# Optimization experiments

Measured on AMD Instinct MI355X. Metric: run time of the kernel, lower is better.

## Reference

```python
import jax, jax.numpy as jnp
import numpy as np

NUM_HEADS = 6

def setup_inputs() -> dict:
    key = jax.random.key(0)
    k1, k2, k3, k4 = jax.random.split(key, 4)
    B, T, C = 128, 256, 384
    s = 1.0 / np.sqrt(C)
    return {
        'x': jax.random.normal(k1, (B, T, C), dtype=jnp.float32),
        'Wq': jax.random.normal(k2, (C, C), dtype=jnp.float32) * s,
        'Wk': jax.random.normal(k3, (C, C), dtype=jnp.float32) * s,
        'Wv': jax.random.normal(k4, (C, C), dtype=jnp.float32) * s,
    }

def reference(x, Wq, Wk, Wv):
    B, T, C = x.shape
    H = NUM_HEADS
    d = C // H
    # projections (bias-free Linear), split into heads
    q = (x @ Wq).reshape(B, T, H, d)
    k = (x @ Wk).reshape(B, T, H, d)
    v = (x @ Wv).reshape(B, T, H, d)
    # NOTE: original scales by 1/sqrt(C), not 1/sqrt(head_dim)
    scale = 1.0 / jnp.sqrt(jnp.asarray(C, dtype=x.dtype))
    att = jnp.einsum('bqhd,bkhd->bhqk', q, k) * scale  # [B,H,T,T]
    causal = jnp.tril(jnp.ones((T, T), dtype=bool))
    att = jnp.where(causal, att, -jnp.inf)
    att = jax.nn.softmax(att, axis=-1)
    # dropout is identity in eval/deterministic mode
    out = jnp.einsum('bhqk,bkhd->bqhd', att, v)  # [B,T,H,d]
    return out.reshape(B, T, C)
```

## Files before the change

kernel.cpp:

```cpp
#include <hip/hip_runtime.h>


typedef unsigned short u16;
typedef float f32x4 __attribute__((ext_vector_type(4)));
typedef short s16x8 __attribute__((ext_vector_type(8)));

static constexpr int BB = 128;
static constexpr int TT = 256;
static constexpr int CC = 384;
static constexpr int HH = 6;
static constexpr int DD = 64;
static constexpr int MM = BB * TT;

static constexpr size_t WTOFF = 0;
static constexpr size_t XOFF  = (size_t)3 * CC * CC;

static constexpr float CSC = 0.07362242194579907f;

__device__ __forceinline__ u16 f2bf(float f) {
  unsigned u = __float_as_uint(f);
  u += 0x7fffu + ((u >> 16) & 1u);
  return (u16)(u >> 16);
}

__device__ __forceinline__ void g2l16(const u16* g, u16* l) {
  __builtin_amdgcn_global_load_lds(
      (const __attribute__((address_space(1))) u16*)g,
      (__attribute__((address_space(3))) u16*)l, 16, 0, 0);
}

__global__ void prep(const float* __restrict__ X, const float* __restrict__ Wq,
                     const float* __restrict__ Wk, const float* __restrict__ Wv,
                     u16* __restrict__ ws) {
  int bx = blockIdx.x;
  if (bx < 6144) {
    size_t i = (size_t)(bx * 256 + threadIdx.x) * 8;
    f32x4 a0 = *(const f32x4*)(X + i);
    f32x4 a1 = *(const f32x4*)(X + i + 4);
    s16x8 ab;
#pragma unroll
    for (int j = 0; j < 4; ++j) { ab[j] = (short)f2bf(a0[j]); ab[4 + j] = (short)f2bf(a1[j]); }
    *(s16x8*)(ws + XOFF + i) = ab;
  } else {
    int j = bx - 6144;
    int z = j / 576;
    const float* W = (z == 0) ? Wq : (z == 1) ? Wk : Wv;
    const float sc = (z == 0) ? CSC : 1.0f;
    u16* WT = ws + WTOFF + (size_t)z * CC * CC;
    int i = (j % 576) * 256 + threadIdx.x;
    int k = i / CC, n = i % CC;
    WT[(size_t)n * CC + k] = f2bf(W[i] * sc);
  }
}

__global__ __launch_bounds__(512, 2) void fused(const u16* __restrict__ ws,
                                                float* __restrict__ out) {
  const int bid = blockIdx.x;
  const int xc = bid & 7;
  const int g5 = bid >> 3;
  const int b = xc * 16 + g5 / 6;
  const int h = g5 % 6;

  __shared__ u16 Xs[256][64];
  __shared__ u16 Ws[192][64];
  __shared__ u16 Ks[256][64];
  __shared__ u16 VTs[64][256];

  const int tid = threadIdx.x;
  const int lane = tid & 63;
  const int w = tid >> 6;
  const int quad = lane >> 4;
  const int col = lane & 15;

  const u16* Xg = ws + XOFF + (size_t)b * TT * CC;
  const u16* Wg = ws + WTOFF;

  const int rl = lane >> 3;
  const int gb = (lane & 7) ^ rl;

  const int wm = (w >> 1) * 64;
  const int wn = (w & 1) * 96;

  f32x4 acc[4][6] = {};

  for (int kt = 0; kt < 6; ++kt) {
    if (kt) __syncthreads();
#pragma unroll
    for (int i = 0; i < 4; ++i) {
      int r0 = w * 32 + i * 8;
      g2l16(Xg + (size_t)(r0 + rl) * CC + kt * 64 + gb * 8, &Xs[r0][0]);
    }
#pragma unroll
    for (int i = 0; i < 3; ++i) {
      int r0 = w * 24 + i * 8;
      int rr = r0 + rl;
      int z = rr >> 6, nn = rr & 63;
      g2l16(Wg + (size_t)(z * CC + h * DD + nn) * CC + kt * 64 + gb * 8, &Ws[r0][0]);
    }
    __syncthreads();

    s16x8 af[4][2];
#pragma unroll
    for (int mt = 0; mt < 4; ++mt)
#pragma unroll
      for (int ks = 0; ks < 2; ++ks)
        af[mt][ks] = *(const s16x8*)(&Xs[wm + mt * 16 + col]
                                        [(((ks * 4 + quad) ^ (col & 7)) * 8)]);
#pragma unroll
    for (int nt = 0; nt < 6; ++nt) {
      s16x8 bf[2];
#pragma unroll
      for (int ks = 0; ks < 2; ++ks)
        bf[ks] = *(const s16x8*)(&Ws[wn + nt * 16 + col]
                                    [(((ks * 4 + quad) ^ (col & 7)) * 8)]);
#pragma unroll
      for (int ks = 0; ks < 2; ++ks)
#pragma unroll
        for (int mt = 0; mt < 4; ++mt)
          acc[mt][nt] = __builtin_amdgcn_mfma_f32_16x16x32_bf16(
              af[mt][ks], bf[ks], acc[mt][nt], 0, 0, 0);
    }
  }
  __syncthreads();

#pragma unroll
  for (int mt = 0; mt < 4; ++mt) {
    int tokb = wm + mt * 16 + quad * 4;
#pragma unroll
    for (int nt = 0; nt < 6; ++nt) {
      int gn = wn + nt * 16 + col;
      if (gn < 128) {
        u16* dst = (gn < 64) ? (u16*)Xs : (u16*)Ks;
        int d = gn & 63;
#pragma unroll
        for (int r = 0; r < 4; ++r) {
          int tok = tokb + r;
          dst[tok * 64 + (d ^ ((tok & 7) << 3))] = f2bf(acc[mt][nt][r]);
        }
      } else {
        int d = gn - 128;
        uint2 pk;
        pk.x = (unsigned)f2bf(acc[mt][nt][0]) | ((unsigned)f2bf(acc[mt][nt][1]) << 16);
        pk.y = (unsigned)f2bf(acc[mt][nt][2]) | ((unsigned)f2bf(acc[mt][nt][3]) << 16);
        *(uint2*)((u16*)VTs + d * 256 + (tokb ^ ((d & 15) << 3))) = pk;
      }
    }
  }
  __syncthreads();

  u16* Ps = (u16*)Ws + (size_t)w * 1152 + (size_t)col * 72;

  s16x8 qf[2][2];
#pragma unroll
  for (int gi = 0; gi < 2; ++gi) {
    int g = gi ? (15 - w) : w;
    int q = g * 16 + col;
#pragma unroll
    for (int ks = 0; ks < 2; ++ks)
      qf[gi][ks] = *(const s16x8*)((u16*)Xs + q * 64 +
                                   (((ks * 4 + quad) ^ (q & 7)) << 3));
  }

  f32x4 o[2][4] = {};
  float mst[2] = {-1.0e30f, -1.0e30f}, lst[2] = {0.0f, 0.0f};

  const int kthi = (15 - w) >> 2;
  for (int kt = 0; kt <= kthi; ++kt) {
    s16x8 kf[4][2], vf[4][2];
#pragma unroll
    for (int nt = 0; nt < 4; ++nt)
#pragma unroll
      for (int ks = 0; ks < 2; ++ks) {
        int key = kt * 64 + nt * 16 + col;
        kf[nt][ks] = *(const s16x8*)((u16*)Ks + key * 64 +
                                     (((ks * 4 + quad) ^ (key & 7)) << 3));
        int d = nt * 16 + col;
        vf[nt][ks] = *(const s16x8*)((u16*)VTs + d * 256 +
                                     ((kt * 64 + ks * 32 + quad * 8) ^ ((d & 15) << 3)));
      }

#pragma unroll
    for (int gi = 0; gi < 2; ++gi) {
      const int g = gi ? (15 - w) : w;
      const int gmax = g >> 2;
      if (kt > gmax) continue;

      f32x4 s[4] = {};
#pragma unroll
      for (int ks = 0; ks < 2; ++ks)
#pragma unroll
        for (int nt = 0; nt < 4; ++nt)
          s[nt] = __builtin_amdgcn_mfma_f32_16x16x32_bf16(kf[nt][ks], qf[gi][ks],
                                                          s[nt], 0, 0, 0);

      const int qq = (g & 3) * 16 + col;
      const bool diag = (kt == gmax);
      float rmax = -1.0e30f;
#pragma unroll
      for (int nt = 0; nt < 4; ++nt)
#pragma unroll
        for (int r = 0; r < 4; ++r) {
          float t = s[nt][r];
          if (diag && (nt * 16 + quad * 4 + r) > qq) t = -1.0e30f;
          s[nt][r] = t;
          rmax = fmaxf(rmax, t);
        }
      rmax = fmaxf(rmax, __shfl_xor(rmax, 16));
      rmax = fmaxf(rmax, __shfl_xor(rmax, 32));

      float mn = fmaxf(mst[gi], rmax);
      float alpha = exp2f(mst[gi] - mn);
      mst[gi] = mn;

      float lsum = 0.0f;
      unsigned pk[4][2];
#pragma unroll
      for (int nt = 0; nt < 4; ++nt) {
        float p0 = exp2f(s[nt][0] - mn), p1 = exp2f(s[nt][1] - mn);
        float p2 = exp2f(s[nt][2] - mn), p3 = exp2f(s[nt][3] - mn);
        lsum += (p0 + p1) + (p2 + p3);
        pk[nt][0] = (unsigned)f2bf(p0) | ((unsigned)f2bf(p1) << 16);
        pk[nt][1] = (unsigned)f2bf(p2) | ((unsigned)f2bf(p3) << 16);
      }
      lst[gi] = lst[gi] * alpha + lsum;

#pragma unroll
      for (int dt = 0; dt < 4; ++dt)
#pragma unroll
        for (int r = 0; r < 4; ++r) o[gi][dt][r] *= alpha;

      asm volatile("s_waitcnt lgkmcnt(0)" ::: "memory");
#pragma unroll
      for (int nt = 0; nt < 4; ++nt)
        *(uint2*)(Ps + nt * 16 + quad * 4) = make_uint2(pk[nt][0], pk[nt][1]);
      asm volatile("s_waitcnt lgkmcnt(0)" ::: "memory");

      s16x8 pf[2];
#pragma unroll
      for (int ks = 0; ks < 2; ++ks)
        pf[ks] = *(const s16x8*)(Ps + ks * 32 + quad * 8);

#pragma unroll
      for (int ks = 0; ks < 2; ++ks)
#pragma unroll
        for (int dt = 0; dt < 4; ++dt)
          o[gi][dt] = __builtin_amdgcn_mfma_f32_16x16x32_bf16(vf[dt][ks], pf[ks],
                                                              o[gi][dt], 0, 0, 0);
    }
  }

#pragma unroll
  for (int gi = 0; gi < 2; ++gi) {
    int g = gi ? (15 - w) : w;
    float l = lst[gi];
    l += __shfl_xor(l, 16);
    l += __shfl_xor(l, 32);
    float inv = 1.0f / l;
    int q = g * 16 + col;
#pragma unroll
    for (int dt = 0; dt < 4; ++dt) {
      f32x4 res;
#pragma unroll
      for (int r = 0; r < 4; ++r) res[r] = o[gi][dt][r] * inv;
      *(f32x4*)(out + (size_t)(b * TT + q) * CC + h * DD + dt * 16 + quad * 4) = res;
    }
  }
}

extern "C" void kernel_launch(void* const* d_in, const int* in_sizes, int n_in,
                              void* d_out, int out_size, void* d_ws, size_t ws_size,
                              hipStream_t stream) {
  const float* x  = (const float*)d_in[0];
  const float* wq = (const float*)d_in[1];
  const float* wk = (const float*)d_in[2];
  const float* wv = (const float*)d_in[3];
  u16* ws  = (u16*)d_ws;
  float* out = (float*)d_out;

  prep<<<dim3(6144 + 1728), 256, 0, stream>>>(x, wq, wk, wv, ws);
  fused<<<dim3(BB * HH), 512, 0, stream>>>(ws, out);
}
```

Baseline: 159.6 us.

## Double threads per block, pipeline projection loads, tile weight transpose via LDS

New measurement: 167.2 us. 4.7% more time.

```diff
diff --git a/kernel.cpp b/kernel.cpp
--- a/kernel.cpp
+++ b/kernel.cpp
@@ -4,6 +4,7 @@
 typedef unsigned short u16;
 typedef float f32x4 __attribute__((ext_vector_type(4)));
 typedef short s16x8 __attribute__((ext_vector_type(8)));
+typedef u16 u16x4 __attribute__((ext_vector_type(4)));
 
 static constexpr int BB = 128;
 static constexpr int TT = 256;
@@ -42,27 +43,43 @@
     for (int j = 0; j < 4; ++j) { ab[j] = (short)f2bf(a0[j]); ab[4 + j] = (short)f2bf(a1[j]); }
     *(s16x8*)(ws + XOFF + i) = ab;
   } else {
+    __shared__ u16 Lt[64][66];
     int j = bx - 6144;
-    int z = j / 576;
+    int z = j / 36, t = j % 36, ti = t / 6, tj = t % 6;
     const float* W = (z == 0) ? Wq : (z == 1) ? Wk : Wv;
     const float sc = (z == 0) ? CSC : 1.0f;
     u16* WT = ws + WTOFF + (size_t)z * CC * CC;
-    int i = (j % 576) * 256 + threadIdx.x;
-    int k = i / CC, n = i % CC;
-    WT[(size_t)n * CC + k] = f2bf(W[i] * sc);
-  }
-}
-
-__global__ __launch_bounds__(512, 2) void fused(const u16* __restrict__ ws,
-                                                float* __restrict__ out) {
+    const int rl = threadIdx.x >> 4;
+    const int cl = (threadIdx.x & 15) * 4;
+#pragma unroll
+    for (int it = 0; it < 4; ++it) {
+      int r = it * 16 + rl;
+      f32x4 v = *(const f32x4*)(W + (size_t)(ti * 64 + r) * CC + tj * 64 + cl);
+#pragma unroll
+      for (int q = 0; q < 4; ++q) Lt[r][cl + q] = f2bf(v[q] * sc);
+    }
+    __syncthreads();
+#pragma unroll
+    for (int it = 0; it < 4; ++it) {
+      int n = it * 16 + rl;
+      u16x4 o;
+#pragma unroll
+      for (int q = 0; q < 4; ++q) o[q] = Lt[cl + q][n];
+      *(u16x4*)(WT + (size_t)(tj * 64 + n) * CC + ti * 64 + cl) = o;
+    }
+  }
+}
+
+__global__ __launch_bounds__(1024, 4) void fused(const u16* __restrict__ ws,
+                                                 float* __restrict__ out) {
   const int bid = blockIdx.x;
   const int xc = bid & 7;
   const int g5 = bid >> 3;
   const int b = xc * 16 + g5 / 6;
   const int h = g5 % 6;
 
-  __shared__ u16 Xs[256][64];
-  __shared__ u16 Ws[192][64];
+  __shared__ u16 R1[256][64];
+  __shared__ u16 R2[16][1152];
   __shared__ u16 Ks[256][64];
   __shared__ u16 VTs[64][256];
 
@@ -71,66 +88,84 @@
   const int w = tid >> 6;
   const int quad = lane >> 4;
   const int col = lane & 15;
+  const int a = w >> 2;
+  const int bq = w & 3;
+  const int wm = a * 64;
+  const int wn = bq * 48;
 
   const u16* Xg = ws + XOFF + (size_t)b * TT * CC;
   const u16* Wg = ws + WTOFF;
+  u16* Wst = &R2[0][0];
 
   const int rl = lane >> 3;
   const int gb = (lane & 7) ^ rl;
 
-  const int wm = (w >> 1) * 64;
-  const int wn = (w & 1) * 96;
-
-  f32x4 acc[4][6] = {};
+  auto stage = [&](int kt) {
+    int r0 = w * 16;
+    g2l16(Xg + (size_t)(r0 + rl) * CC + kt * 64 + gb * 8, &R1[r0][0]);
+    g2l16(Xg + (size_t)(r0 + 8 + rl) * CC + kt * 64 + gb * 8, &R1[r0 + 8][0]);
+    {
+      int rr = w * 8 + rl;
+      int z = rr >> 6, nn = rr & 63;
+      g2l16(Wg + (size_t)(z * CC + h * DD + nn) * CC + kt * 64 + gb * 8,
+            Wst + w * 512);
+    }
+    if (w < 8) {
+      int c = w + 16;
+      int rr = c * 8 + rl;
+      int z = rr >> 6, nn = rr & 63;
+      g2l16(Wg + (size_t)(z * CC + h * DD + nn) * CC + kt * 64 + gb * 8,
+            Wst + c * 512);
+    }
+  };
+
+  f32x4 acc[4][3] = {};
+
+  stage(0);
+  asm volatile("s_waitcnt vmcnt(0)" ::: "memory");
+  __syncthreads();
 
   for (int kt = 0; kt < 6; ++kt) {
-    if (kt) __syncthreads();
-#pragma unroll
-    for (int i = 0; i < 4; ++i) {
-      int r0 = w * 32 + i * 8;
-      g2l16(Xg + (size_t)(r0 + rl) * CC + kt * 64 + gb * 8, &Xs[r0][0]);
-    }
-#pragma unroll
-    for (int i = 0; i < 3; ++i) {
-      int r0 = w * 24 + i * 8;
-      int rr = r0 + rl;
-      int z = rr >> 6, nn = rr & 63;
-      g2l16(Wg + (size_t)(z * CC + h * DD + nn) * CC + kt * 64 + gb * 8, &Ws[r0][0]);
-    }
+    s16x8 af[4][2], bf[3][2];
+#pragma unroll
+    for (int mt = 0; mt < 4; ++mt)
+#pragma unroll
+      for (int ks = 0; ks < 2; ++ks)
+        af[mt][ks] = *(const s16x8*)(&R1[wm + mt * 16 + col]
+                                        [(((ks * 4 + quad) ^ (col & 7)) * 8)]);
+#pragma unroll
+    for (int nt = 0; nt < 3; ++nt)
+#pragma unroll
+      for (int ks = 0; ks < 2; ++ks)
+        bf[nt][ks] = *(const s16x8*)(Wst + (wn + nt * 16 + col) * 64 +
+                                     (((ks * 4 + quad) ^ (col & 7)) * 8));
+
     __syncthreads();
-
-    s16x8 af[4][2];
-#pragma unroll
-    for (int mt = 0; mt < 4; ++mt)
-#pragma unroll
-      for (int ks = 0; ks < 2; ++ks)
-        af[mt][ks] = *(const s16x8*)(&Xs[wm + mt * 16 + col]
-                                        [(((ks * 4 + quad) ^ (col & 7)) * 8)]);
-#pragma unroll
-    for (int nt = 0; nt < 6; ++nt) {
-      s16x8 bf[2];
-#pragma unroll
-      for (int ks = 0; ks < 2; ++ks)
-        bf[ks] = *(const s16x8*)(&Ws[wn + nt * 16 + col]
-                                    [(((ks * 4 + quad) ^ (col & 7)) * 8)]);
-#pragma unroll
-      for (int ks = 0; ks < 2; ++ks)
-#pragma unroll
-        for (int mt = 0; mt < 4; ++mt)
+    if (kt < 5) stage(kt + 1);
+
+#pragma unroll
+    for (int ks = 0; ks < 2; ++ks)
+#pragma unroll
+      for (int mt = 0; mt < 4; ++mt)
+#pragma unroll
+        for (int nt = 0; nt < 3; ++nt)
           acc[mt][nt] = __builtin_amdgcn_mfma_f32_16x16x32_bf16(
-              af[mt][ks], bf[ks], acc[mt][nt], 0, 0, 0);
-    }
-  }
-  __syncthreads();
+              af[mt][ks], bf[nt][ks], acc[mt][nt], 0, 0, 0);
+
+    if (kt < 5) {
+      asm volatile("s_waitcnt vmcnt(0)" ::: "memory");
+      __syncthreads();
+    }
+  }
 
 #pragma unroll
   for (int mt = 0; mt < 4; ++mt) {
     int tokb = wm + mt * 16 + quad * 4;
 #pragma unroll
-    for (int nt = 0; nt < 6; ++nt) {
+    for (int nt = 0; nt < 3; ++nt) {
       int gn = wn + nt * 16 + col;
       if (gn < 128) {
-        u16* dst = (gn < 64) ? (u16*)Xs : (u16*)Ks;
+        u16* dst = (gn < 64) ? &R1[0][0] : &Ks[0][0];
         int d = gn & 63;
 #pragma unroll
         for (int r = 0; r < 4; ++r) {
@@ -148,23 +183,23 @@
   }
   __syncthreads();
 
-  u16* Ps = (u16*)Ws + (size_t)w * 1152 + (size_t)col * 72;
-
-  s16x8 qf[2][2];
-#pragma unroll
-  for (int gi = 0; gi < 2; ++gi) {
-    int g = gi ? (15 - w) : w;
+  const int gcl = (a + bq) & 3;
+  const int g = gcl * 4 + a;
+  const int kthi = g >> 2;
+  const int qq = (g & 3) * 16 + col;
+  u16* Ps = &R2[w][col * 72];
+
+  s16x8 qf[2];
+  {
     int q = g * 16 + col;
 #pragma unroll
     for (int ks = 0; ks < 2; ++ks)
-      qf[gi][ks] = *(const s16x8*)((u16*)Xs + q * 64 +
-                                   (((ks * 4 + quad) ^ (q & 7)) << 3));
-  }
-
-  f32x4 o[2][4] = {};
-  float mst[2] = {-1.0e30f, -1.0e30f}, lst[2] = {0.0f, 0.0f};
-
-  const int kthi = (15 - w) >> 2;
+      qf[ks] = *(const s16x8*)(&R1[q][(((ks * 4 + quad) ^ (q & 7)) * 8)]);
+  }
+
+  f32x4 o[4] = {};
+  float mst = -1.0e30f, lst = 0.0f;
+
   for (int kt = 0; kt <= kthi; ++kt) {
     s16x8 kf[4][2], vf[4][2];
 #pragma unroll
@@ -172,87 +207,76 @@
 #pragma unroll
       for (int ks = 0; ks < 2; ++ks) {
         int key = kt * 64 + nt * 16 + col;
-        kf[nt][ks] = *(const s16x8*)((u16*)Ks + key * 64 +
-                                     (((ks * 4 + quad) ^ (key & 7)) << 3));
+        kf[nt][ks] = *(const s16x8*)(&Ks[key][(((ks * 4 + quad) ^ (col & 7)) * 8)]);
         int d = nt * 16 + col;
-        vf[nt][ks] = *(const s16x8*)((u16*)VTs + d * 256 +
-                                     ((kt * 64 + ks * 32 + quad * 8) ^ ((d & 15) << 3)));
+        vf[nt][ks] = *(const s16x8*)((const u16*)VTs + d * 256 +
+                     ((kt * 64 + ks * 32 + quad * 8) ^ ((d & 15) << 3)));
       }
 
-#pragma unroll
-    for (int gi = 0; gi < 2; ++gi) {
-      const int g = gi ? (15 - w) : w;
-      const int gmax = g >> 2;
-      if (kt > gmax) continue;
-
-      f32x4 s[4] = {};
-#pragma unroll
-      for (int ks = 0; ks < 2; ++ks)
-#pragma unroll
-        for (int nt = 0; nt < 4; ++nt)
-          s[nt] = __builtin_amdgcn_mfma_f32_16x16x32_bf16(kf[nt][ks], qf[gi][ks],
-                                                          s[nt], 0, 0, 0);
-
-      const int qq = (g & 3) * 16 + col;
-      const bool diag = (kt == gmax);
-      float rmax = -1.0e30f;
+    f32x4 s[4] = {};
+#pragma unroll
+    for (int ks = 0; ks < 2; ++ks)
 #pragma unroll
       for (int nt = 0; nt < 4; ++nt)
-#pragma unroll
-        for (int r = 0; r < 4; ++r) {
-          float t = s[nt][r];
-          if (diag && (nt * 16 + quad * 4 + r) > qq) t = -1.0e30f;
-          s[nt][r] = t;
-          rmax = fmaxf(rmax, t);
-        }
-      rmax = fmaxf(rmax, __shfl_xor(rmax, 16));
-      rmax = fmaxf(rmax, __shfl_xor(rmax, 32));
-
-      float mn = fmaxf(mst[gi], rmax);
-      float alpha = exp2f(mst[gi] - mn);
-      mst[gi] = mn;
-
-      float lsum = 0.0f;
-      unsigned pk[4][2];
-#pragma unroll
-      for (int nt = 0; nt < 4; ++nt) {
-        float p0 = exp2f(s[nt][0] - mn), p1 = exp2f(s[nt][1] - mn);
-        float p2 = exp2f(s[nt][2] - mn), p3 = exp2f(s[nt][3] - mn);
-        lsum += (p0 + p1) + (p2 + p3);
-        pk[nt][0] = (unsigned)f2bf(p0) | ((unsigned)f2bf(p1) << 16);
-        pk[nt][1] = (unsigned)f2bf(p2) | ((unsigned)f2bf(p3) << 16);
+        s[nt] = __builtin_amdgcn_mfma_f32_16x16x32_bf16(kf[nt][ks], qf[ks],
+                                                        s[nt], 0, 0, 0);
+
+    const bool diag = (kt == kthi);
+    float rmax = -1.0e30f;
+#pragma unroll
+    for (int nt = 0; nt < 4; ++nt)
+#pragma unroll
+      for (int r = 0; r < 4; ++r) {
+        float t = s[nt][r];
+        if (diag && (nt * 16 + quad * 4 + r) > qq) t = -1.0e30f;
+        s[nt][r] = t;
+        rmax = fmaxf(rmax, t);
       }
-      lst[gi] = lst[gi] * alpha + lsum;
-
+    rmax = fmaxf(rmax, __shfl_xor(rmax, 16));
+    rmax = fmaxf(rmax, __shfl_xor(rmax, 32));
+
+    float mn = fmaxf(mst, rmax);
+    float alpha = exp2f(mst - mn);
+    mst = mn;
+
+    float lsum = 0.0f;
+    unsigned pk[4][2];
+#pragma unroll
+    for (int nt = 0; nt < 4; ++nt) {
+      float p0 = exp2f(s[nt][0] - mn), p1 = exp2f(s[nt][1] - mn);
+      float p2 = exp2f(s[nt][2] - mn), p3 = exp2f(s[nt][3] - mn);
+      lsum += (p0 + p1) + (p2 + p3);
+      pk[nt][0] = (unsigned)f2bf(p0) | ((unsigned)f2bf(p1) << 16);
+      pk[nt][1] = (unsigned)f2bf(p2) | ((unsigned)f2bf(p3) << 16);
+    }
+    lst = lst * alpha + lsum;
+
+    asm volatile("s_waitcnt lgkmcnt(0)" ::: "memory");
+#pragma unroll
+    for (int nt = 0; nt < 4; ++nt)
+      *(uint2*)(Ps + nt * 16 + quad * 4) = make_uint2(pk[nt][0], pk[nt][1]);
+
+#pragma unroll
+    for (int dt = 0; dt < 4; ++dt)
+#pragma unroll
+      for (int r = 0; r < 4; ++r) o[dt][r] *= alpha;
+
+    asm volatile("s_waitcnt lgkmcnt(0)" ::: "memory");
+    s16x8 pf[2];
+#pragma unroll
+    for (int ks = 0; ks < 2; ++ks)
+      pf[ks] = *(const s16x8*)(Ps + ks * 32 + quad * 8);
+
+#pragma unroll
+    for (int ks = 0; ks < 2; ++ks)
 #pragma unroll
       for (int dt = 0; dt < 4; ++dt)
-#pragma unroll
-        for (int r = 0; r < 4; ++r) o[gi][dt][r] *= alpha;
-
-      asm volatile("s_waitcnt lgkmcnt(0)" ::: "memory");
-#pragma unroll
-      for (int nt = 0; nt < 4; ++nt)
-        *(uint2*)(Ps + nt * 16 + quad * 4) = make_uint2(pk[nt][0], pk[nt][1]);
-      asm volatile("s_waitcnt lgkmcnt(0)" ::: "memory");
-
-      s16x8 pf[2];
-#pragma unroll
-      for (int ks = 0; ks < 2; ++ks)
-        pf[ks] = *(const s16x8*)(Ps + ks * 32 + quad * 8);
-
-#pragma unroll
-      for (int ks = 0; ks < 2; ++ks)
-#pragma unroll
-        for (int dt = 0; dt < 4; ++dt)
-          o[gi][dt] = __builtin_amdgcn_mfma_f32_16x16x32_bf16(vf[dt][ks], pf[ks],
-                                                              o[gi][dt], 0, 0, 0);
-    }
-  }
-
-#pragma unroll
-  for (int gi = 0; gi < 2; ++gi) {
-    int g = gi ? (15 - w) : w;
-    float l = lst[gi];
+        o[dt] = __builtin_amdgcn_mfma_f32_16x16x32_bf16(vf[dt][ks], pf[ks],
+                                                        o[dt], 0, 0, 0);
+  }
+
+  {
+    float l = lst;
     l += __shfl_xor(l, 16);
     l += __shfl_xor(l, 32);
     float inv = 1.0f / l;
@@ -261,7 +285,7 @@
     for (int dt = 0; dt < 4; ++dt) {
       f32x4 res;
 #pragma unroll
-      for (int r = 0; r < 4; ++r) res[r] = o[gi][dt][r] * inv;
+      for (int r = 0; r < 4; ++r) res[r] = o[dt][r] * inv;
       *(f32x4*)(out + (size_t)(b * TT + q) * CC + h * DD + dt * 16 + quad * 4) = res;
     }
   }
@@ -277,6 +301,6 @@
   u16* ws  = (u16*)d_ws;
   float* out = (float*)d_out;
 
-  prep<<<dim3(6144 + 1728), 256, 0, stream>>>(x, wq, wk, wv, ws);
-  fused<<<dim3(BB * HH), 512, 0, stream>>>(ws, out);
-}
+  prep<<<dim3(6144 + 108), 256, 0, stream>>>(x, wq, wk, wv, ws);
+  fused<<<dim3(BB * HH), 1024, 0, stream>>>(ws, out);
+}
```
